# Kernel optimization log

Hardware: AMD Instinct MI355X
Metric: run time of the kernel (lower is better)

## Reference

```python
import jax, jax.numpy as jnp
import numpy as np

VOCAB, EMB_DIM, HIDDEN, NUM_CLASSES = 100000, 128, 256, 20
B, S = 4096, 200


def setup_inputs() -> dict:
    key = jax.random.key(0)
    k1, k2, k3, k4, k5, k6, k7 = jax.random.split(key, 7)
    x = jax.random.randint(k1, (B, S), 0, VOCAB, dtype=jnp.int64)
    seq_lengths = jnp.maximum(jax.random.randint(k2, (B,), 0, S, dtype=jnp.int64), 1)
    emb = jax.random.normal(k3, (VOCAB, EMB_DIM), dtype=jnp.float32) * 0.02
    emb = emb.at[0].set(0.0)  # padding_idx=0
    W1 = jax.random.normal(k4, (EMB_DIM, HIDDEN), dtype=jnp.float32) * (1.0 / np.sqrt(EMB_DIM))
    b1 = jax.random.normal(k5, (HIDDEN,), dtype=jnp.float32) * 0.01
    W2 = jax.random.normal(k6, (HIDDEN, NUM_CLASSES), dtype=jnp.float32) * (1.0 / np.sqrt(HIDDEN))
    b2 = jax.random.normal(k7, (NUM_CLASSES,), dtype=jnp.float32) * 0.01
    return {"x": x, "seq_lengths": seq_lengths, "emb": emb, "W1": W1, "b1": b1, "W2": W2, "b2": b2}


def reference(x, seq_lengths, emb, W1, b1, W2, b2):
    # Embedding lookup: [B, S, D]
    e = emb[x]
    # Masked mean over first seq_lengths[i] positions (fused, no per-sample loop)
    mask = (jnp.arange(S)[None, :] < seq_lengths[:, None]).astype(e.dtype)  # [B, S]
    pooled = jnp.einsum('bsd,bs->bd', e, mask) / seq_lengths[:, None].astype(e.dtype)
    # MLP (dropout is identity in eval mode)
    hidden = jax.nn.relu(pooled @ W1 + b1)
    return hidden @ W2 + b2
```

## Files before the change

kernel.cpp:

```cpp
#include <hip/hip_runtime.h>

#define B 4096
#define S 200
#define EMB_DIM 128
#define HIDDEN 256
#define NUM_CLASSES 20
#define VOCAB 100000
#define RB 4

typedef __attribute__((ext_vector_type(8))) unsigned short ushort8;

__device__ __forceinline__ unsigned short f2bf(float f) {
    unsigned u = __float_as_uint(f);
    unsigned r = u + 0x7fffu + ((u >> 16) & 1u);
    return (unsigned short)(r >> 16);
}

__global__ __launch_bounds__(256) void convert_kernel(
    const float* __restrict__ emb,
    unsigned short* __restrict__ embh)
{
    const long i = ((long)blockIdx.x * 256 + threadIdx.x) * 8;
    const float4 a = *(const float4*)(emb + i);
    const float4 b = *(const float4*)(emb + i + 4);
    ushort8 o;
    o[0] = f2bf(a.x); o[1] = f2bf(a.y); o[2] = f2bf(a.z); o[3] = f2bf(a.w);
    o[4] = f2bf(b.x); o[5] = f2bf(b.y); o[6] = f2bf(b.z); o[7] = f2bf(b.w);
    *(ushort8*)(embh + i) = o;
}

__global__ __launch_bounds__(256, 4) void fused_kernel(
    const int* __restrict__ x,
    const int* __restrict__ lens,
    const unsigned short* __restrict__ embh,
    const float* __restrict__ W1,
    const float* __restrict__ b1,
    const float* __restrict__ W2,
    const float* __restrict__ b2,
    float* __restrict__ out)
{
    __shared__ int   sidx[RB][256];
    __shared__ float tmp[2][16][16][8];
    __shared__ float P[RB][EMB_DIM];
    __shared__ float H[RB][HIDDEN];
    __shared__ float part[RB][2][NUM_CLASSES];

    const int t  = threadIdx.x;
    const int b0 = blockIdx.x * RB;

    int Ls[RB];
    #pragma unroll
    for (int r = 0; r < RB; ++r) {
        Ls[r] = lens[b0 + r];
        int v = 0;
        if (t < Ls[r]) v = x[(long)(b0 + r) * S + t];
        sidx[r][t] = v;
    }
    __syncthreads();

    const int g   = t >> 4;
    const int d   = t & 15;
    const int dof = d << 3;

    float acc[RB][8];
    #pragma unroll
    for (int r = 0; r < RB; ++r)
        #pragma unroll
        for (int f = 0; f < 8; ++f) acc[r][f] = 0.f;

    #pragma unroll
    for (int pair = 0; pair < 2; ++pair) {
        const int na   = (Ls[pair * 2]     + 63) >> 6;
        const int nb   = (Ls[pair * 2 + 1] + 63) >> 6;
        const int nMax = na > nb ? na : nb;

        int cur[2][4], nxt[2][4];
        #pragma unroll
        for (int p = 0; p < 2; ++p)
            #pragma unroll
            for (int j = 0; j < 4; ++j)
                cur[p][j] = sidx[pair * 2 + p][g + 16 * j];

        for (int it = 0; it < nMax; ++it) {
            uint4 v[2][4];
            #pragma unroll
            for (int p = 0; p < 2; ++p)
                #pragma unroll
                for (int j = 0; j < 4; ++j)
                    v[p][j] = *(const uint4*)(embh + ((cur[p][j] << 7) + dof));

            const int nb2 = ((it + 1) & 3) << 6;
            #pragma unroll
            for (int p = 0; p < 2; ++p)
                #pragma unroll
                for (int j = 0; j < 4; ++j)
                    nxt[p][j] = sidx[pair * 2 + p][nb2 + g + 16 * j];

            #pragma unroll
            for (int p = 0; p < 2; ++p)
                #pragma unroll
                for (int j = 0; j < 4; ++j) {
                    const unsigned c0 = v[p][j].x, c1 = v[p][j].y;
                    const unsigned c2 = v[p][j].z, c3 = v[p][j].w;
                    acc[pair * 2 + p][0] += __uint_as_float(c0 << 16);
                    acc[pair * 2 + p][1] += __uint_as_float(c0 & 0xffff0000u);
                    acc[pair * 2 + p][2] += __uint_as_float(c1 << 16);
                    acc[pair * 2 + p][3] += __uint_as_float(c1 & 0xffff0000u);
                    acc[pair * 2 + p][4] += __uint_as_float(c2 << 16);
                    acc[pair * 2 + p][5] += __uint_as_float(c2 & 0xffff0000u);
                    acc[pair * 2 + p][6] += __uint_as_float(c3 << 16);
                    acc[pair * 2 + p][7] += __uint_as_float(c3 & 0xffff0000u);
                }

            #pragma unroll
            for (int p = 0; p < 2; ++p)
                #pragma unroll
                for (int j = 0; j < 4; ++j) cur[p][j] = nxt[p][j];
        }
    }

    #pragma unroll
    for (int half = 0; half < 2; ++half) {
        if (half) __syncthreads();
        #pragma unroll
        for (int rr = 0; rr < 2; ++rr)
            #pragma unroll
            for (int f = 0; f < 8; ++f)
                tmp[rr][g][d][f] = acc[half * 2 + rr][f];
        __syncthreads();
        {
            const int rr  = t >> 7;
            const int dim = t & 127;
            float s = 0.f;
            #pragma unroll
            for (int gg = 0; gg < 16; ++gg) s += tmp[rr][gg][dim >> 3][dim & 7];
            const float L = rr ? (float)Ls[half * 2 + 1] : (float)Ls[half * 2];
            P[half * 2 + rr][dim] = s / L;
        }
    }
    __syncthreads();

    {
        float hA[RB], hB[RB];
        #pragma unroll
        for (int r = 0; r < RB; ++r) { hA[r] = 0.f; hB[r] = 0.f; }
        for (int k = 0; k < EMB_DIM; k += 2) {
            const float wa = W1[(k)     * HIDDEN + t];
            const float wb = W1[(k + 1) * HIDDEN + t];
            #pragma unroll
            for (int r = 0; r < RB; ++r) {
                hA[r] = fmaf(P[r][k],     wa, hA[r]);
                hB[r] = fmaf(P[r][k + 1], wb, hB[r]);
            }
        }
        const float bb = b1[t];
        #pragma unroll
        for (int r = 0; r < RB; ++r)
            H[r][t] = fmaxf(hA[r] + hB[r] + bb, 0.f);
    }
    __syncthreads();

    if (t < RB * 2 * NUM_CLASSES) {
        const int r  = t / (2 * NUM_CLASSES);
        const int u  = t - r * 2 * NUM_CLASSES;
        const int j  = u / NUM_CLASSES;
        const int c  = u - j * NUM_CLASSES;
        const int k0 = j * 128;
        float a0 = 0.f, a1 = 0.f;
        for (int k = k0; k < k0 + 128; k += 2) {
            a0 = fmaf(H[r][k],     W2[(k)     * NUM_CLASSES + c], a0);
            a1 = fmaf(H[r][k + 1], W2[(k + 1) * NUM_CLASSES + c], a1);
        }
        part[r][j][c] = a0 + a1;
    }
    __syncthreads();

    if (t < RB * NUM_CLASSES) {
        const int r = t / NUM_CLASSES;
        const int c = t - r * NUM_CLASSES;
        out[(long)(b0 + r) * NUM_CLASSES + c] =
            b2[c] + part[r][0][c] + part[r][1][c];
    }
}

extern "C" void kernel_launch(void* const* d_in, const int* in_sizes, int n_in,
                              void* d_out, int out_size, void* d_ws, size_t ws_size,
                              hipStream_t stream) {
    const int*   x    = (const int*)d_in[0];
    const int*   lens = (const int*)d_in[1];
    const float* emb  = (const float*)d_in[2];
    const float* W1   = (const float*)d_in[3];
    const float* b1   = (const float*)d_in[4];
    const float* W2   = (const float*)d_in[5];
    const float* b2   = (const float*)d_in[6];
    float*       out  = (float*)d_out;

    unsigned short* embh = (unsigned short*)d_ws;

    convert_kernel<<<(VOCAB * EMB_DIM) / (8 * 256), 256, 0, stream>>>(emb, embh);
    fused_kernel<<<B / RB, 256, 0, stream>>>(x, lens, embh, W1, b1, W2, b2, out);
}
```

Measured before the change: 125.0 us.

## Quantize embedding table to int8 with per-row scales for gather

Replaces the bf16 conversion of the embedding table with per-row symmetric int8 quantization plus a float scale per row. The fused kernel then gathers 128-byte rows, dequantizing with an FMA, and threads are remapped to cover 16 dims each. This halves gathered bytes and conversion writes, at the cost of extra scale loads and lower numeric precision.

After: 123.1 us. About the same (-1.5%).

```diff
diff --git a/kernel.cpp b/kernel.cpp
--- a/kernel.cpp
+++ b/kernel.cpp
@@ -8,31 +8,38 @@
 #define VOCAB 100000
 #define RB 4
 
-typedef __attribute__((ext_vector_type(8))) unsigned short ushort8;
-
-__device__ __forceinline__ unsigned short f2bf(float f) {
-    unsigned u = __float_as_uint(f);
-    unsigned r = u + 0x7fffu + ((u >> 16) & 1u);
-    return (unsigned short)(r >> 16);
+__global__ __launch_bounds__(256) void convert_q8(
+    const float* __restrict__ emb,
+    signed char* __restrict__ qt,
+    float* __restrict__ scl)
+{
+    const int  t    = threadIdx.x;
+    const long base = (long)blockIdx.x * 1024 + t * 4;
+    const float4 v  = *(const float4*)(emb + base);
+
+    float m = fmaxf(fmaxf(fabsf(v.x), fabsf(v.y)),
+                    fmaxf(fabsf(v.z), fabsf(v.w)));
+    #pragma unroll
+    for (int off = 1; off < 32; off <<= 1)
+        m = fmaxf(m, __shfl_xor(m, off, 64));
+
+    const float inv = m > 0.f ? 127.f / m : 0.f;
+    const int q0 = __float2int_rn(v.x * inv);
+    const int q1 = __float2int_rn(v.y * inv);
+    const int q2 = __float2int_rn(v.z * inv);
+    const int q3 = __float2int_rn(v.w * inv);
+    const unsigned pk = (q0 & 255) | ((q1 & 255) << 8)
+                      | ((q2 & 255) << 16) | ((q3 & 255) << 24);
+    *(unsigned*)(qt + base) = pk;
+
+    if ((t & 31) == 0) scl[base >> 7] = m * (1.f / 127.f);
 }
 
-__global__ __launch_bounds__(256) void convert_kernel(
-    const float* __restrict__ emb,
-    unsigned short* __restrict__ embh)
-{
-    const long i = ((long)blockIdx.x * 256 + threadIdx.x) * 8;
-    const float4 a = *(const float4*)(emb + i);
-    const float4 b = *(const float4*)(emb + i + 4);
-    ushort8 o;
-    o[0] = f2bf(a.x); o[1] = f2bf(a.y); o[2] = f2bf(a.z); o[3] = f2bf(a.w);
-    o[4] = f2bf(b.x); o[5] = f2bf(b.y); o[6] = f2bf(b.z); o[7] = f2bf(b.w);
-    *(ushort8*)(embh + i) = o;
-}
-
-__global__ __launch_bounds__(256, 4) void fused_kernel(
+__global__ __launch_bounds__(256) void fused_kernel(
     const int* __restrict__ x,
     const int* __restrict__ lens,
-    const unsigned short* __restrict__ embh,
+    const signed char* __restrict__ qt,
+    const float* __restrict__ scl,
     const float* __restrict__ W1,
     const float* __restrict__ b1,
     const float* __restrict__ W2,
@@ -40,7 +47,7 @@
     float* __restrict__ out)
 {
     __shared__ int   sidx[RB][256];
-    __shared__ float tmp[2][16][16][8];
+    __shared__ float tmp[32][8][16];
     __shared__ float P[RB][EMB_DIM];
     __shared__ float H[RB][HIDDEN];
     __shared__ float part[RB][2][NUM_CLASSES];
@@ -58,15 +65,9 @@
     }
     __syncthreads();
 
-    const int g   = t >> 4;
-    const int d   = t & 15;
-    const int dof = d << 3;
-
-    float acc[RB][8];
-    #pragma unroll
-    for (int r = 0; r < RB; ++r)
-        #pragma unroll
-        for (int f = 0; f < 8; ++f) acc[r][f] = 0.f;
+    const int g   = t >> 3;
+    const int d   = t & 7;
+    const int dof = d << 4;
 
     #pragma unroll
     for (int pair = 0; pair < 2; ++pair) {
@@ -74,68 +75,73 @@
         const int nb   = (Ls[pair * 2 + 1] + 63) >> 6;
         const int nMax = na > nb ? na : nb;
 
-        int cur[2][4], nxt[2][4];
+        float acc[2][16];
         #pragma unroll
         for (int p = 0; p < 2; ++p)
             #pragma unroll
-            for (int j = 0; j < 4; ++j)
-                cur[p][j] = sidx[pair * 2 + p][g + 16 * j];
+            for (int f = 0; f < 16; ++f) acc[p][f] = 0.f;
+
+        int cur[2][2], nxt[2][2];
+        #pragma unroll
+        for (int p = 0; p < 2; ++p)
+            #pragma unroll
+            for (int j = 0; j < 2; ++j)
+                cur[p][j] = sidx[pair * 2 + p][(j << 5) + g];
 
         for (int it = 0; it < nMax; ++it) {
-            uint4 v[2][4];
-            #pragma unroll
-            for (int p = 0; p < 2; ++p)
-                #pragma unroll
-                for (int j = 0; j < 4; ++j)
-                    v[p][j] = *(const uint4*)(embh + ((cur[p][j] << 7) + dof));
+            uint4 v[2][2];
+            float s[2][2];
+            #pragma unroll
+            for (int p = 0; p < 2; ++p)
+                #pragma unroll
+                for (int j = 0; j < 2; ++j) {
+                    v[p][j] = *(const uint4*)(qt + ((cur[p][j] << 7) + dof));
+                    s[p][j] = scl[cur[p][j]];
+                }
 
             const int nb2 = ((it + 1) & 3) << 6;
             #pragma unroll
             for (int p = 0; p < 2; ++p)
                 #pragma unroll
-                for (int j = 0; j < 4; ++j)
-                    nxt[p][j] = sidx[pair * 2 + p][nb2 + g + 16 * j];
-
-            #pragma unroll
-            for (int p = 0; p < 2; ++p)
-                #pragma unroll
-                for (int j = 0; j < 4; ++j) {
-                    const unsigned c0 = v[p][j].x, c1 = v[p][j].y;
-                    const unsigned c2 = v[p][j].z, c3 = v[p][j].w;
-                    acc[pair * 2 + p][0] += __uint_as_float(c0 << 16);
-                    acc[pair * 2 + p][1] += __uint_as_float(c0 & 0xffff0000u);
-                    acc[pair * 2 + p][2] += __uint_as_float(c1 << 16);
-                    acc[pair * 2 + p][3] += __uint_as_float(c1 & 0xffff0000u);
-                    acc[pair * 2 + p][4] += __uint_as_float(c2 << 16);
-                    acc[pair * 2 + p][5] += __uint_as_float(c2 & 0xffff0000u);
-                    acc[pair * 2 + p][6] += __uint_as_float(c3 << 16);
-                    acc[pair * 2 + p][7] += __uint_as_float(c3 & 0xffff0000u);
+                for (int j = 0; j < 2; ++j)
+                    nxt[p][j] = sidx[pair * 2 + p][nb2 + (j << 5) + g];
+
+            #pragma unroll
+            for (int p = 0; p < 2; ++p)
+                #pragma unroll
+                for (int j = 0; j < 2; ++j) {
+                    const float sc = s[p][j];
+                    #pragma unroll
+                    for (int w = 0; w < 4; ++w) {
+                        const unsigned c = w == 0 ? v[p][j].x : w == 1 ? v[p][j].y
+                                         : w == 2 ? v[p][j].z : v[p][j].w;
+                        acc[p][w * 4 + 0] = fmaf(sc, (float)((int)(c << 24) >> 24), acc[p][w * 4 + 0]);
+                        acc[p][w * 4 + 1] = fmaf(sc, (float)((int)(c << 16) >> 24), acc[p][w * 4 + 1]);
+                        acc[p][w * 4 + 2] = fmaf(sc, (float)((int)(c <<  8) >> 24), acc[p][w * 4 + 2]);
+                        acc[p][w * 4 + 3] = fmaf(sc, (float)((int)(c      ) >> 24), acc[p][w * 4 + 3]);
+                    }
                 }
 
             #pragma unroll
             for (int p = 0; p < 2; ++p)
                 #pragma unroll
-                for (int j = 0; j < 4; ++j) cur[p][j] = nxt[p][j];
-        }
-    }
-
-    #pragma unroll
-    for (int half = 0; half < 2; ++half) {
-        if (half) __syncthreads();
-        #pragma unroll
-        for (int rr = 0; rr < 2; ++rr)
-            #pragma unroll
-            for (int f = 0; f < 8; ++f)
-                tmp[rr][g][d][f] = acc[half * 2 + rr][f];
-        __syncthreads();
-        {
-            const int rr  = t >> 7;
-            const int dim = t & 127;
-            float s = 0.f;
-            #pragma unroll
-            for (int gg = 0; gg < 16; ++gg) s += tmp[rr][gg][dim >> 3][dim & 7];
-            const float L = rr ? (float)Ls[half * 2 + 1] : (float)Ls[half * 2];
-            P[half * 2 + rr][dim] = s / L;
+                for (int j = 0; j < 2; ++j) cur[p][j] = nxt[p][j];
+        }
+
+        #pragma unroll
+        for (int rr = 0; rr < 2; ++rr) {
+            if (pair || rr) __syncthreads();
+            #pragma unroll
+            for (int f = 0; f < 16; ++f)
+                tmp[g][d][f] = acc[rr][f];
+            __syncthreads();
+            if (t < 128) {
+                float ssum = 0.f;
+                #pragma unroll
+                for (int gg = 0; gg < 32; ++gg)
+                    ssum += tmp[gg][t >> 4][t & 15];
+                P[pair * 2 + rr][t] = ssum / (float)Ls[pair * 2 + rr];
+            }
         }
     }
     __syncthreads();
@@ -195,8 +201,9 @@
     const float* b2   = (const float*)d_in[6];
     float*       out  = (float*)d_out;
 
-    unsigned short* embh = (unsigned short*)d_ws;
-
-    convert_kernel<<<(VOCAB * EMB_DIM) / (8 * 256), 256, 0, stream>>>(emb, embh);
-    fused_kernel<<<B / RB, 256, 0, stream>>>(x, lens, embh, W1, b1, W2, b2, out);
+    signed char* qt  = (signed char*)d_ws;
+    float*       scl = (float*)((char*)d_ws + (16l << 20));
+
+    convert_q8<<<(VOCAB * EMB_DIM) / (4 * 256), 256, 0, stream>>>(emb, qt, scl);
+    fused_kernel<<<B / RB, 256, 0, stream>>>(x, lens, qt, scl, W1, b1, W2, b2, out);
 }
```

## Drop bf16 table conversion pass and gather fp32 embeddings directly

Applied to the files above, without the earlier changes.

Removes the per-call kernel that converts the whole fp32 embedding table to bf16, and has the fused kernel gather fp32 rows directly. Each thread now handles 4 floats per 16-byte load, so 32 lanes cover a row and 8 token groups run per row. The cross-group reduction through shared memory is simplified to match. This trades the full-table read and write of the conversion pass for twice the bytes per gathered token, and it also restores fp32 accuracy.

Result: no change. 125.2 us (+0.2%).

```diff
diff --git a/kernel.cpp b/kernel.cpp
--- a/kernel.cpp
+++ b/kernel.cpp
@@ -8,31 +8,10 @@
 #define VOCAB 100000
 #define RB 4
 
-typedef __attribute__((ext_vector_type(8))) unsigned short ushort8;
-
-__device__ __forceinline__ unsigned short f2bf(float f) {
-    unsigned u = __float_as_uint(f);
-    unsigned r = u + 0x7fffu + ((u >> 16) & 1u);
-    return (unsigned short)(r >> 16);
-}
-
-__global__ __launch_bounds__(256) void convert_kernel(
-    const float* __restrict__ emb,
-    unsigned short* __restrict__ embh)
-{
-    const long i = ((long)blockIdx.x * 256 + threadIdx.x) * 8;
-    const float4 a = *(const float4*)(emb + i);
-    const float4 b = *(const float4*)(emb + i + 4);
-    ushort8 o;
-    o[0] = f2bf(a.x); o[1] = f2bf(a.y); o[2] = f2bf(a.z); o[3] = f2bf(a.w);
-    o[4] = f2bf(b.x); o[5] = f2bf(b.y); o[6] = f2bf(b.z); o[7] = f2bf(b.w);
-    *(ushort8*)(embh + i) = o;
-}
-
 __global__ __launch_bounds__(256, 4) void fused_kernel(
     const int* __restrict__ x,
     const int* __restrict__ lens,
-    const unsigned short* __restrict__ embh,
+    const float* __restrict__ emb,
     const float* __restrict__ W1,
     const float* __restrict__ b1,
     const float* __restrict__ W2,
@@ -40,7 +19,7 @@
     float* __restrict__ out)
 {
     __shared__ int   sidx[RB][256];
-    __shared__ float tmp[2][16][16][8];
+    __shared__ float tmp[RB][8][EMB_DIM];
     __shared__ float P[RB][EMB_DIM];
     __shared__ float H[RB][HIDDEN];
     __shared__ float part[RB][2][NUM_CLASSES];
@@ -58,20 +37,20 @@
     }
     __syncthreads();
 
-    const int g   = t >> 4;
-    const int d   = t & 15;
-    const int dof = d << 3;
+    const int g   = t >> 5;
+    const int d   = t & 31;
+    const int dof = d << 2;
 
-    float acc[RB][8];
+    float acc[RB][4];
     #pragma unroll
     for (int r = 0; r < RB; ++r)
         #pragma unroll
-        for (int f = 0; f < 8; ++f) acc[r][f] = 0.f;
+        for (int f = 0; f < 4; ++f) acc[r][f] = 0.f;
 
     #pragma unroll
     for (int pair = 0; pair < 2; ++pair) {
-        const int na   = (Ls[pair * 2]     + 63) >> 6;
-        const int nb   = (Ls[pair * 2 + 1] + 63) >> 6;
+        const int na   = (Ls[pair * 2]     + 31) >> 5;
+        const int nb   = (Ls[pair * 2 + 1] + 31) >> 5;
         const int nMax = na > nb ? na : nb;
 
         int cur[2][4], nxt[2][4];
@@ -79,37 +58,31 @@
         for (int p = 0; p < 2; ++p)
             #pragma unroll
             for (int j = 0; j < 4; ++j)
-                cur[p][j] = sidx[pair * 2 + p][g + 16 * j];
+                cur[p][j] = sidx[pair * 2 + p][(j << 3) + g];
 
         for (int it = 0; it < nMax; ++it) {
-            uint4 v[2][4];
+            float4 v[2][4];
             #pragma unroll
             for (int p = 0; p < 2; ++p)
                 #pragma unroll
                 for (int j = 0; j < 4; ++j)
-                    v[p][j] = *(const uint4*)(embh + ((cur[p][j] << 7) + dof));
+                    v[p][j] = *(const float4*)(emb + ((long)(cur[p][j] << 7) + dof));
 
-            const int nb2 = ((it + 1) & 3) << 6;
+            const int nb2 = (it + 1) << 5;
             #pragma unroll
             for (int p = 0; p < 2; ++p)
                 #pragma unroll
                 for (int j = 0; j < 4; ++j)
-                    nxt[p][j] = sidx[pair * 2 + p][nb2 + g + 16 * j];
+                    nxt[p][j] = sidx[pair * 2 + p][((nb2 + (j << 3) + g) & 255)];
 
             #pragma unroll
             for (int p = 0; p < 2; ++p)
                 #pragma unroll
                 for (int j = 0; j < 4; ++j) {
-                    const unsigned c0 = v[p][j].x, c1 = v[p][j].y;
-                    const unsigned c2 = v[p][j].z, c3 = v[p][j].w;
-                    acc[pair * 2 + p][0] += __uint_as_float(c0 << 16);
-                    acc[pair * 2 + p][1] += __uint_as_float(c0 & 0xffff0000u);
-                    acc[pair * 2 + p][2] += __uint_as_float(c1 << 16);
-                    acc[pair * 2 + p][3] += __uint_as_float(c1 & 0xffff0000u);
-                    acc[pair * 2 + p][4] += __uint_as_float(c2 << 16);
-                    acc[pair * 2 + p][5] += __uint_as_float(c2 & 0xffff0000u);
-                    acc[pair * 2 + p][6] += __uint_as_float(c3 << 16);
-                    acc[pair * 2 + p][7] += __uint_as_float(c3 & 0xffff0000u);
+                    acc[pair * 2 + p][0] += v[p][j].x;
+                    acc[pair * 2 + p][1] += v[p][j].y;
+                    acc[pair * 2 + p][2] += v[p][j].z;
+                    acc[pair * 2 + p][3] += v[p][j].w;
                 }
 
             #pragma unroll
@@ -120,23 +93,18 @@
     }
 
     #pragma unroll
-    for (int half = 0; half < 2; ++half) {
-        if (half) __syncthreads();
+    for (int r = 0; r < RB; ++r)
+        *(float4*)&tmp[r][g][dof] = *(float4*)acc[r];
+    __syncthreads();
+
+    #pragma unroll
+    for (int pass = 0; pass < 2; ++pass) {
+        const int r   = pass * 2 + (t >> 7);
+        const int dim = t & 127;
+        float s = 0.f;
         #pragma unroll
-        for (int rr = 0; rr < 2; ++rr)
-            #pragma unroll
-            for (int f = 0; f < 8; ++f)
-                tmp[rr][g][d][f] = acc[half * 2 + rr][f];
-        __syncthreads();
-        {
-            const int rr  = t >> 7;
-            const int dim = t & 127;
-            float s = 0.f;
-            #pragma unroll
-            for (int gg = 0; gg < 16; ++gg) s += tmp[rr][gg][dim >> 3][dim & 7];
-            const float L = rr ? (float)Ls[half * 2 + 1] : (float)Ls[half * 2];
-            P[half * 2 + rr][dim] = s / L;
-        }
+        for (int gg = 0; gg < 8; ++gg) s += tmp[r][gg][dim];
+        P[r][dim] = s / (float)Ls[r];
     }
     __syncthreads();
 
@@ -195,8 +163,5 @@
     const float* b2   = (const float*)d_in[6];
     float*       out  = (float*)d_out;
 
-    unsigned short* embh = (unsigned short*)d_ws;
-
-    convert_kernel<<<(VOCAB * EMB_DIM) / (8 * 256), 256, 0, stream>>>(emb, embh);
-    fused_kernel<<<B / RB, 256, 0, stream>>>(x, lens, embh, W1, b1, W2, b2, out);
+    fused_kernel<<<B / RB, 256, 0, stream>>>(x, lens, emb, W1, b1, W2, b2, out);
 }
```
